# Performance work log

Hardware: AMD Instinct MI355X
Metric: run time of the kernel (lower is better)

Reference implementation:

```python
import jax, jax.numpy as jnp
import numpy as np

B, I, H = 512, 2048, 2048


def setup_inputs() -> dict:
    key = jax.random.key(0)
    ks = jax.random.split(key, 14)
    s = 0.02  # weight init scale
    inp = {
        "inputs": jax.random.normal(ks[0], (B, I), jnp.float32),
        "states": jax.random.normal(ks[1], (2, B, H), jnp.float32),
        "Wi": jax.random.normal(ks[2], (I, H), jnp.float32) * s,
        "Ui": jax.random.normal(ks[3], (H, H), jnp.float32) * s,
        "bi": jnp.zeros((H,), jnp.float32),
        "Wf": jax.random.normal(ks[4], (I, H), jnp.float32) * s,
        "Uf": jax.random.normal(ks[5], (H, H), jnp.float32) * s,
        "bf": jnp.zeros((H,), jnp.float32),
        "Wg": jax.random.normal(ks[6], (I, H), jnp.float32) * s,
        "Ug": jax.random.normal(ks[7], (H, H), jnp.float32) * s,
        "bg": jnp.zeros((H,), jnp.float32),
        "Wc": jax.random.normal(ks[8], (I, H), jnp.float32) * s,
        "Uc": jax.random.normal(ks[9], (H, H), jnp.float32) * s,
        "bc": jnp.zeros((H,), jnp.float32),
    }
    return inp


def reference(inputs, states, Wi, Ui, bi, Wf, Uf, bf, Wg, Ug, bg, Wc, Uc, bc):
    # Faithful to the original cell, including its quirks:
    # recurrent matmuls use states[0] (prevstate); c mixes states[1] (prevoutput).
    prevstate, prevoutput = states[0], states[1]  # [B,H] each
    i = jax.nn.sigmoid(inputs @ Wi + prevstate @ Ui + bi)
    f = jax.nn.sigmoid(inputs @ Wf + prevstate @ Uf + bf)
    g = jax.nn.sigmoid(inputs @ Wg + prevstate @ Ug + bg)
    c_ = jnp.tanh(inputs @ Wc + prevstate @ Uc + bc)
    c = f * prevoutput + i * c_
    state = g * jnp.tanh(c)
    return c, jnp.stack([state, c])
```

## Files before the change

### kernel.cpp

```cpp
#include <hip/hip_runtime.h>

#define BH (512*2048)
#define BHA 1048576ull
#define PPLANE (512ull*8192ull)
#define PLANE_BYTES (PPLANE*2ull)
#define AB_ELEMS (2ull*512*2048)

typedef __attribute__((ext_vector_type(8))) short short8;
typedef __attribute__((ext_vector_type(4))) float floatx4;
typedef __attribute__((ext_vector_type(4))) unsigned int uint4v;
typedef __attribute__((ext_vector_type(8))) unsigned short ushort8v;

__device__ inline unsigned pk2(float a, float b){
    unsigned ua = __builtin_bit_cast(unsigned, a) + 0x8000u;
    unsigned ub = __builtin_bit_cast(unsigned, b) + 0x8000u;
    return __builtin_amdgcn_perm(ub, ua, 0x07060302u);
}
__device__ inline unsigned short f2bf1(float x){
    return (unsigned short)((__builtin_bit_cast(unsigned, x) + 0x8000u) >> 16);
}
__device__ inline float bf2f(unsigned short s){
    return __builtin_bit_cast(float, ((unsigned)s) << 16);
}
__device__ inline int swz(int r, int g){ return r*4 + (g ^ ((r>>1)&3)); }
__device__ inline float fsig(float x){ return __builtin_amdgcn_rcpf(1.f + __expf(-x)); }
__device__ inline float ftanh(float x){ return 2.f*fsig(2.f*x) - 1.f; }

__global__ __launch_bounds__(256) void prep_act(
    const float* __restrict__ inputs, const float* __restrict__ states,
    unsigned short* __restrict__ Ab)
{
    const size_t off = ((size_t)blockIdx.x * 256 + threadIdx.x) * 8;
    const float* src = (off < BHA) ? (inputs + off) : (states + (off - BHA));
    floatx4 v0 = *(const floatx4*)src;
    floatx4 v1 = *(const floatx4*)(src + 4);
    uint4v w;
    w.x = pk2(v0[0],v0[1]); w.y = pk2(v0[2],v0[3]);
    w.z = pk2(v1[0],v1[1]); w.w = pk2(v1[2],v1[3]);
    *(uint4v*)(Ab + off) = w;
}

__global__ __launch_bounds__(256, 3) void gemm_fused(
    const float* __restrict__ Wi, const float* __restrict__ Ui,
    const float* __restrict__ Wf, const float* __restrict__ Uf,
    const float* __restrict__ Wg, const float* __restrict__ Ug,
    const float* __restrict__ Wc, const float* __restrict__ Uc,
    const unsigned short* __restrict__ Ab, unsigned short* __restrict__ P)
{
    __shared__ unsigned short As[2][4096];
    __shared__ unsigned short Bs[2][4096];

    const int t = threadIdx.x, lane = t & 63, wave = t >> 6;
    const int nblk = blockIdx.x, gate = nblk >> 4, nb = nblk & 15;
    const int m0 = blockIdx.y * 128, z = blockIdx.z;

    const float* Bsel;
    if (z < 2) { switch (gate){ case 0: Bsel=Wi; break; case 1: Bsel=Wf; break;
                                case 2: Bsel=Wg; break; default: Bsel=Wc; } }
    else       { switch (gate){ case 0: Bsel=Ui; break; case 1: Bsel=Uf; break;
                                case 2: Bsel=Ug; break; default: Bsel=Uc; } }
    const int n   = t & 127;
    const int o0  = t >> 7;
    const int swkB = (n >> 1) & 3;
    const float* Bp0 = Bsel + ((size_t)((z & 1) * 1024 + o0 * 8)) * 2048
                            + nb * 128 + n;
    const float* Bp1 = Bp0 + (size_t)16 * 2048;
    const int wb0 = n * 32 + (((o0    ) ^ swkB) << 3);
    const int wb1 = n * 32 + (((o0 + 2) ^ swkB) << 3);

    const int ar = t >> 1, ah = t & 1;
    const int swkA = (ar >> 1) & 3;
    const unsigned short* Aptr = Ab + (size_t)(z >> 1) * BHA
                               + (size_t)(m0 + ar) * 2048 + (z & 1) * 1024
                               + ah * 16;
    const int wa0 = ar * 32 + (((2*ah    ) ^ swkA) << 3);
    const int wa1 = ar * 32 + (((2*ah + 1) ^ swkA) << 3);

    floatx4 acc[4][4];
    #pragma unroll
    for (int i = 0; i < 4; i++)
        #pragma unroll
        for (int j = 0; j < 4; j++)
            acc[i][j] = (floatx4){0.f,0.f,0.f,0.f};

    const int wm = (wave & 1) * 64, wn = (wave >> 1) * 64;
    const int row16 = lane & 15, g4 = lane >> 4;
    const int fgx = ((g4 ^ ((row16 >> 1) & 3)) << 3);

    float uB0a[8], uB0b[8], uB1a[8], uB1b[8];
    uint4v uA0a, uA0b, uA1a, uA1b;

#define B_LOAD(d0, d1, tile) do { \
    const float* q0_ = Bp0 + (size_t)(tile) * 65536; \
    const float* q1_ = Bp1 + (size_t)(tile) * 65536; \
    _Pragma("unroll") for (int j = 0; j < 8; j++) d0[j] = q0_[(size_t)j * 2048]; \
    _Pragma("unroll") for (int j = 0; j < 8; j++) d1[j] = q1_[(size_t)j * 2048]; \
} while(0)

#define B_WRITE(buf, s0, s1) do { \
    *(uint4v*)&Bs[buf][wb0] = (uint4v){pk2(s0[0],s0[1]), pk2(s0[2],s0[3]), \
                                       pk2(s0[4],s0[5]), pk2(s0[6],s0[7])}; \
    *(uint4v*)&Bs[buf][wb1] = (uint4v){pk2(s1[0],s1[1]), pk2(s1[2],s1[3]), \
                                       pk2(s1[4],s1[5]), pk2(s1[6],s1[7])}; \
} while(0)

#define A_LOAD(da, db, tile) do { \
    const unsigned short* ap_ = Aptr + (size_t)(tile) * 32; \
    da = *(const uint4v*)ap_; db = *(const uint4v*)(ap_ + 8); \
} while(0)

#define A_WRITE(buf, sa, sb) do { \
    *(uint4v*)&As[buf][wa0] = sa; *(uint4v*)&As[buf][wa1] = sb; \
} while(0)

#define FRAGS_MFMA(buf) do { \
    short8 afr[4], bfr[4]; \
    _Pragma("unroll") for (int mi = 0; mi < 4; mi++) \
        afr[mi] = *(const short8*)&As[buf][(wm + mi*16 + row16)*32 + fgx]; \
    _Pragma("unroll") for (int ni = 0; ni < 4; ni++) \
        bfr[ni] = *(const short8*)&Bs[buf][(wn + ni*16 + row16)*32 + fgx]; \
    _Pragma("unroll") for (int mi = 0; mi < 4; mi++) \
        _Pragma("unroll") for (int ni = 0; ni < 4; ni++) \
            acc[mi][ni] = __builtin_amdgcn_mfma_f32_16x16x32_bf16( \
                afr[mi], bfr[ni], acc[mi][ni], 0, 0, 0); \
} while(0)

#define PIPE_BARRIER() do { \
    asm volatile("s_waitcnt lgkmcnt(0)" ::: "memory"); \
    __builtin_amdgcn_s_barrier(); \
    __builtin_amdgcn_sched_barrier(0); \
} while(0)

    A_LOAD(uA0a, uA0b, 0); B_LOAD(uB0a, uB0b, 0);
    A_LOAD(uA1a, uA1b, 1); B_LOAD(uB1a, uB1b, 1);
    A_WRITE(0, uA0a, uA0b);
    B_WRITE(0, uB0a, uB0b);
    PIPE_BARRIER();

    for (int kk = 0; kk < 32; kk += 2) {
        if (kk < 30) { A_LOAD(uA0a, uA0b, kk + 2); B_LOAD(uB0a, uB0b, kk + 2); }
        FRAGS_MFMA(0);
        A_WRITE(1, uA1a, uA1b);
        B_WRITE(1, uB1a, uB1b);
        PIPE_BARRIER();
        if (kk < 30) { A_LOAD(uA1a, uA1b, kk + 3); B_LOAD(uB1a, uB1b, kk + 3); }
        FRAGS_MFMA(1);
        if (kk < 30) {
            A_WRITE(0, uA0a, uA0b);
            B_WRITE(0, uB0a, uB0b);
        }
        PIPE_BARRIER();
    }

#undef B_LOAD
#undef B_WRITE
#undef A_LOAD
#undef A_WRITE
#undef FRAGS_MFMA
#undef PIPE_BARRIER

    unsigned short* dst = P + (size_t)z * PPLANE;
    const int gbase = gate * 2048 + nb * 128;
    #pragma unroll
    for (int mi = 0; mi < 4; mi++)
        #pragma unroll
        for (int ni = 0; ni < 4; ni++)
            #pragma unroll
            for (int j = 0; j < 4; j++) {
                int row = m0 + wm + mi*16 + g4*4 + j;
                int col = gbase + wn + ni*16 + row16;
                dst[(size_t)row * 8192 + col] = f2bf1(acc[mi][ni][j]);
            }
}

__global__ __launch_bounds__(256, 2) void gemm_tile(
    const float* __restrict__ inputs, const float* __restrict__ states,
    const float* __restrict__ Wi, const float* __restrict__ Ui,
    const float* __restrict__ Wf, const float* __restrict__ Uf,
    const float* __restrict__ Wg, const float* __restrict__ Ug,
    const float* __restrict__ Wc, const float* __restrict__ Uc,
    unsigned short* __restrict__ P, int KB)
{
    __shared__ uint4v As[2][512];
    __shared__ uint4v Bs[2][512];

    const int t = threadIdx.x;
    const int m0 = blockIdx.y * 128;
    const int z = blockIdx.z;
    const int nblk = blockIdx.x;
    const int gate = nblk >> 4;
    const int c0 = (nblk & 15) * 128;
    const int gk = z * KB;

    const float* Abase; const float* Bsel; int ko;
    if (gk < 2048) {
        Abase = inputs; ko = gk;
        switch (gate){ case 0: Bsel=Wi; break; case 1: Bsel=Wf; break;
                       case 2: Bsel=Wg; break; default: Bsel=Wc; }
    } else {
        Abase = states; ko = gk - 2048;
        switch (gate){ case 0: Bsel=Ui; break; case 1: Bsel=Uf; break;
                       case 2: Bsel=Ug; break; default: Bsel=Uc; }
    }
    const int NIT = KB >> 5;

    const int lane = t & 63, wave = t >> 6;
    const int wm = (wave & 1) * 64, wn = (wave >> 1) * 64;
    const int row16 = lane & 15, g4 = lane >> 4;
    const int ar = t >> 2, ag = t & 3;
    const int bn = t & 127, bg2 = (t >> 7) * 2;

    const float* Ap = Abase + (size_t)(m0 + ar) * 2048 + ko + ag * 8;
    const float* Bp = Bsel + (size_t)ko * 2048 + c0 + bn;

    floatx4 acc[4][4];
    #pragma unroll
    for (int i = 0; i < 4; i++)
        #pragma unroll
        for (int j = 0; j < 4; j++)
            acc[i][j] = (floatx4){0.f,0.f,0.f,0.f};

    floatx4 a0,a1,a2,a3; float b0[8], b1[8];
    a0 = *(const floatx4*)Ap;             a1 = *(const floatx4*)(Ap + 4);
    a2 = *(const floatx4*)(Ap + 64*2048); a3 = *(const floatx4*)(Ap + 64*2048 + 4);
    #pragma unroll
    for (int j = 0; j < 8; j++) b0[j] = Bp[(size_t)(bg2*8 + j) * 2048];
    #pragma unroll
    for (int j = 0; j < 8; j++) b1[j] = Bp[(size_t)(bg2*8 + 8 + j) * 2048];
    {
        uint4v w;
        w.x=pk2(a0[0],a0[1]); w.y=pk2(a0[2],a0[3]); w.z=pk2(a1[0],a1[1]); w.w=pk2(a1[2],a1[3]);
        As[0][swz(ar, ag)] = w;
        w.x=pk2(a2[0],a2[1]); w.y=pk2(a2[2],a2[3]); w.z=pk2(a3[0],a3[1]); w.w=pk2(a3[2],a3[3]);
        As[0][swz(ar+64, ag)] = w;
        w.x=pk2(b0[0],b0[1]); w.y=pk2(b0[2],b0[3]); w.z=pk2(b0[4],b0[5]); w.w=pk2(b0[6],b0[7]);
        Bs[0][swz(bn, bg2)] = w;
        w.x=pk2(b1[0],b1[1]); w.y=pk2(b1[2],b1[3]); w.z=pk2(b1[4],b1[5]); w.w=pk2(b1[6],b1[7]);
        Bs[0][swz(bn, bg2+1)] = w;
    }

    for (int kk = 0; kk < NIT; kk++) {
        __syncthreads();
        const int cur = kk & 1;
        if (kk + 1 < NIT) {
            const float* ap = Ap + (kk+1) * 32;
            a0 = *(const floatx4*)ap;             a1 = *(const floatx4*)(ap + 4);
            a2 = *(const floatx4*)(ap + 64*2048); a3 = *(const floatx4*)(ap + 64*2048 + 4);
            const float* bp = Bp + (size_t)(kk+1) * 32 * 2048;
            #pragma unroll
            for (int j = 0; j < 8; j++) b0[j] = bp[(size_t)(bg2*8 + j) * 2048];
            #pragma unroll
            for (int j = 0; j < 8; j++) b1[j] = bp[(size_t)(bg2*8 + 8 + j) * 2048];
        }
        short8 afr[4], bfr[4];
        #pragma unroll
        for (int mi = 0; mi < 4; mi++)
            afr[mi] = *(const short8*)&As[cur][swz(wm + mi*16 + row16, g4)];
        #pragma unroll
        for (int ni = 0; ni < 4; ni++)
            bfr[ni] = *(const short8*)&Bs[cur][swz(wn + ni*16 + row16, g4)];
        #pragma unroll
        for (int mi = 0; mi < 4; mi++)
            #pragma unroll
            for (int ni = 0; ni < 4; ni++)
                acc[mi][ni] = __builtin_amdgcn_mfma_f32_16x16x32_bf16(
                    afr[mi], bfr[ni], acc[mi][ni], 0, 0, 0);
        if (kk + 1 < NIT) {
            const int nxt = cur ^ 1;
            uint4v w;
            w.x=pk2(a0[0],a0[1]); w.y=pk2(a0[2],a0[3]); w.z=pk2(a1[0],a1[1]); w.w=pk2(a1[2],a1[3]);
            As[nxt][swz(ar, ag)] = w;
            w.x=pk2(a2[0],a2[1]); w.y=pk2(a2[2],a2[3]); w.z=pk2(a3[0],a3[1]); w.w=pk2(a3[2],a3[3]);
            As[nxt][swz(ar+64, ag)] = w;
            w.x=pk2(b0[0],b0[1]); w.y=pk2(b0[2],b0[3]); w.z=pk2(b0[4],b0[5]); w.w=pk2(b0[6],b0[7]);
            Bs[nxt][swz(bn, bg2)] = w;
            w.x=pk2(b1[0],b1[1]); w.y=pk2(b1[2],b1[3]); w.z=pk2(b1[4],b1[5]); w.w=pk2(b1[6],b1[7]);
            Bs[nxt][swz(bn, bg2+1)] = w;
        }
    }

    unsigned short* dst = P + (size_t)z * PPLANE;
    const int gbase = gate * 2048 + c0;
    #pragma unroll
    for (int mi = 0; mi < 4; mi++)
        #pragma unroll
        for (int ni = 0; ni < 4; ni++)
            #pragma unroll
            for (int j = 0; j < 4; j++) {
                int row = m0 + wm + mi*16 + g4*4 + j;
                int col = gbase + wn + ni*16 + row16;
                dst[(size_t)row * 8192 + col] = f2bf1(acc[mi][ni][j]);
            }
}

__global__ __launch_bounds__(256) void combine_kernel(
    float* __restrict__ out, const unsigned short* __restrict__ P,
    const float* __restrict__ states,
    const float* __restrict__ bi, const float* __restrict__ bfv,
    const float* __restrict__ bg, const float* __restrict__ bc, int nz)
{
    const int idx = (blockIdx.x * 256 + threadIdx.x) * 8;
    const int row = idx >> 11;
    const int h = idx & 2047;
    const size_t base = (size_t)row * 8192 + h;

    float xi[8], xf[8], xg[8], xc[8];
    #pragma unroll
    for (int e = 0; e < 8; e++) {
        xi[e] = bi[h+e]; xf[e] = bfv[h+e]; xg[e] = bg[h+e]; xc[e] = bc[h+e];
    }
    for (int z = 0; z < nz; z++) {
        const unsigned short* Pz = P + (size_t)z * PPLANE;
        ushort8v vi = *(const ushort8v*)&Pz[base];
        ushort8v vf = *(const ushort8v*)&Pz[base + 2048];
        ushort8v vg = *(const ushort8v*)&Pz[base + 4096];
        ushort8v vc = *(const ushort8v*)&Pz[base + 6144];
        #pragma unroll
        for (int e = 0; e < 8; e++) {
            xi[e] += bf2f(vi[e]); xf[e] += bf2f(vf[e]);
            xg[e] += bf2f(vg[e]); xc[e] += bf2f(vc[e]);
        }
    }

    const float* po = states + BH;
    floatx4 pov[2];
    pov[0] = *(const floatx4*)&po[idx];
    pov[1] = *(const floatx4*)&po[idx + 4];

    floatx4 vcv[2], vsv[2];
    #pragma unroll
    for (int q = 0; q < 2; q++)
        #pragma unroll
        for (int j = 0; j < 4; j++) {
            int e = q*4 + j;
            float c = fsig(xf[e]) * pov[q][j] + fsig(xi[e]) * ftanh(xc[e]);
            vcv[q][j] = c;
            vsv[q][j] = fsig(xg[e]) * ftanh(c);
        }
    #pragma unroll
    for (int q = 0; q < 2; q++) {
        *(floatx4*)&out[idx + q*4]        = vcv[q];
        *(floatx4*)&out[BH + idx + q*4]   = vsv[q];
        *(floatx4*)&out[2*BH + idx + q*4] = vcv[q];
    }
}

extern "C" void kernel_launch(void* const* d_in, const int* in_sizes, int n_in,
                              void* d_out, int out_size, void* d_ws, size_t ws_size,
                              hipStream_t stream) {
    const float* inputs = (const float*)d_in[0];
    const float* states = (const float*)d_in[1];
    const float* Wi = (const float*)d_in[2];
    const float* Ui = (const float*)d_in[3];
    const float* bi = (const float*)d_in[4];
    const float* Wf = (const float*)d_in[5];
    const float* Uf = (const float*)d_in[6];
    const float* bf = (const float*)d_in[7];
    const float* Wg = (const float*)d_in[8];
    const float* Ug = (const float*)d_in[9];
    const float* bg = (const float*)d_in[10];
    const float* Wc = (const float*)d_in[11];
    const float* Uc = (const float*)d_in[12];
    const float* bc = (const float*)d_in[13];
    float* out = (float*)d_out;

    const size_t need = (AB_ELEMS + 4 * PPLANE) * 2;
    if (ws_size >= need) {
        unsigned short* Ab = (unsigned short*)d_ws;
        unsigned short* P  = Ab + AB_ELEMS;
        prep_act<<<1024, 256, 0, stream>>>(inputs, states, Ab);
        gemm_fused<<<dim3(64, 4, 4), 256, 0, stream>>>(Wi, Ui, Wf, Uf,
                                                       Wg, Ug, Wc, Uc, Ab, P);
        combine_kernel<<<BH / (8 * 256), 256, 0, stream>>>(out, P, states,
                                                           bi, bf, bg, bc, 4);
    } else {
        unsigned short* P = (unsigned short*)d_ws;
        const int nz = (ws_size >= 4 * PLANE_BYTES) ? 4 : 2;
        const int KB = 4096 / nz;
        dim3 grid(64, 4, nz);
        gemm_tile<<<grid, 256, 0, stream>>>(inputs, states, Wi, Ui, Wf, Uf,
                                            Wg, Ug, Wc, Uc, P, KB);
        combine_kernel<<<BH / (8 * 256), 256, 0, stream>>>(out, P, states,
                                                           bi, bf, bg, bc, nz);
    }
}
```

Before: 238.2 us.

## Load A fragments directly from global and widen B loads to float2

Removes the shared-memory staging of the A (activation) tile: each wave now reads its MFMA A-fragments directly from global memory into registers, double-buffered across k-steps. B loads become float2 vectors covering two columns per thread, with a new swizzled LDS write layout. Launch bounds drop from 3 to 2 blocks per CU to make room for the extra registers. The aim is to cut LDS traffic and halve B load instructions. The cost is that A rows are now fetched redundantly by the two waves sharing the same wm, and occupancy is lower.

```diff
diff --git a/kernel.cpp b/kernel.cpp
--- a/kernel.cpp
+++ b/kernel.cpp
@@ -8,6 +8,7 @@
 
 typedef __attribute__((ext_vector_type(8))) short short8;
 typedef __attribute__((ext_vector_type(4))) float floatx4;
+typedef __attribute__((ext_vector_type(2))) float floatx2;
 typedef __attribute__((ext_vector_type(4))) unsigned int uint4v;
 typedef __attribute__((ext_vector_type(8))) unsigned short ushort8v;
 
@@ -40,41 +41,40 @@
     *(uint4v*)(Ab + off) = w;
 }
 
-__global__ __launch_bounds__(256, 3) void gemm_fused(
+__global__ __launch_bounds__(256, 2) void gemm_fused(
     const float* __restrict__ Wi, const float* __restrict__ Ui,
     const float* __restrict__ Wf, const float* __restrict__ Uf,
     const float* __restrict__ Wg, const float* __restrict__ Ug,
     const float* __restrict__ Wc, const float* __restrict__ Uc,
     const unsigned short* __restrict__ Ab, unsigned short* __restrict__ P)
 {
-    __shared__ unsigned short As[2][4096];
     __shared__ unsigned short Bs[2][4096];
 
     const int t = threadIdx.x, lane = t & 63, wave = t >> 6;
-    const int nblk = blockIdx.x, gate = nblk >> 4, nb = nblk & 15;
+    const int nblk = blockIdx.x, gate = nblk >> 4, nbx = nblk & 15;
     const int m0 = blockIdx.y * 128, z = blockIdx.z;
+    const int ko = (z & 1) * 1024;
 
     const float* Bsel;
     if (z < 2) { switch (gate){ case 0: Bsel=Wi; break; case 1: Bsel=Wf; break;
                                 case 2: Bsel=Wg; break; default: Bsel=Wc; } }
     else       { switch (gate){ case 0: Bsel=Ui; break; case 1: Bsel=Uf; break;
                                 case 2: Bsel=Ug; break; default: Bsel=Uc; } }
-    const int n   = t & 127;
-    const int o0  = t >> 7;
-    const int swkB = (n >> 1) & 3;
-    const float* Bp0 = Bsel + ((size_t)((z & 1) * 1024 + o0 * 8)) * 2048
-                            + nb * 128 + n;
-    const float* Bp1 = Bp0 + (size_t)16 * 2048;
-    const int wb0 = n * 32 + (((o0    ) ^ swkB) << 3);
-    const int wb1 = n * 32 + (((o0 + 2) ^ swkB) << 3);
-
-    const int ar = t >> 1, ah = t & 1;
-    const int swkA = (ar >> 1) & 3;
-    const unsigned short* Aptr = Ab + (size_t)(z >> 1) * BHA
-                               + (size_t)(m0 + ar) * 2048 + (z & 1) * 1024
-                               + ah * 16;
-    const int wa0 = ar * 32 + (((2*ah    ) ^ swkA) << 3);
-    const int wa1 = ar * 32 + (((2*ah + 1) ^ swkA) << 3);
+
+    const int n0  = lane * 2;
+    const int oct = wave;
+    const float* Bp = Bsel + (size_t)(ko + oct * 8) * 2048 + nbx * 128 + n0;
+    const int keyB = lane & 3;
+    const int wb0 = n0 * 32 + ((oct ^ keyB) << 3);
+    const int wb1 = wb0 + 32;
+
+    const int wm = (wave & 1) * 64, wn = (wave >> 1) * 64;
+    const int row16 = lane & 15, g4 = lane >> 4;
+    const int fgx = (g4 ^ ((row16 >> 1) & 3)) << 3;
+
+    const unsigned short* Ap = Ab + (size_t)(z >> 1) * BHA
+                             + (size_t)(m0 + wm + row16) * 2048
+                             + (z & 1) * 1024 + g4 * 8;
 
     floatx4 acc[4][4];
     #pragma unroll
@@ -83,84 +83,73 @@
         for (int j = 0; j < 4; j++)
             acc[i][j] = (floatx4){0.f,0.f,0.f,0.f};
 
-    const int wm = (wave & 1) * 64, wn = (wave >> 1) * 64;
-    const int row16 = lane & 15, g4 = lane >> 4;
-    const int fgx = ((g4 ^ ((row16 >> 1) & 3)) << 3);
-
-    float uB0a[8], uB0b[8], uB1a[8], uB1b[8];
-    uint4v uA0a, uA0b, uA1a, uA1b;
-
-#define B_LOAD(d0, d1, tile) do { \
-    const float* q0_ = Bp0 + (size_t)(tile) * 65536; \
-    const float* q1_ = Bp1 + (size_t)(tile) * 65536; \
-    _Pragma("unroll") for (int j = 0; j < 8; j++) d0[j] = q0_[(size_t)j * 2048]; \
-    _Pragma("unroll") for (int j = 0; j < 8; j++) d1[j] = q1_[(size_t)j * 2048]; \
-} while(0)
-
-#define B_WRITE(buf, s0, s1) do { \
-    *(uint4v*)&Bs[buf][wb0] = (uint4v){pk2(s0[0],s0[1]), pk2(s0[2],s0[3]), \
-                                       pk2(s0[4],s0[5]), pk2(s0[6],s0[7])}; \
-    *(uint4v*)&Bs[buf][wb1] = (uint4v){pk2(s1[0],s1[1]), pk2(s1[2],s1[3]), \
-                                       pk2(s1[4],s1[5]), pk2(s1[6],s1[7])}; \
-} while(0)
-
-#define A_LOAD(da, db, tile) do { \
-    const unsigned short* ap_ = Aptr + (size_t)(tile) * 32; \
-    da = *(const uint4v*)ap_; db = *(const uint4v*)(ap_ + 8); \
-} while(0)
-
-#define A_WRITE(buf, sa, sb) do { \
-    *(uint4v*)&As[buf][wa0] = sa; *(uint4v*)&As[buf][wa1] = sb; \
-} while(0)
-
-#define FRAGS_MFMA(buf) do { \
-    short8 afr[4], bfr[4]; \
+    floatx2 q0[8], q1[8];
+    short8 fA[4], fB[4];
+
+#define B_LOAD(d, tile) do { \
+    const float* bp_ = Bp + (size_t)(tile) * 65536; \
+    _Pragma("unroll") for (int j = 0; j < 8; j++) \
+        d[j] = *(const floatx2*)(bp_ + (size_t)j * 2048); \
+} while(0)
+
+#define B_WRITE(buf, s) do { \
+    *(uint4v*)&Bs[buf][wb0] = (uint4v){pk2(s[0].x,s[1].x), pk2(s[2].x,s[3].x), \
+                                       pk2(s[4].x,s[5].x), pk2(s[6].x,s[7].x)}; \
+    *(uint4v*)&Bs[buf][wb1] = (uint4v){pk2(s[0].y,s[1].y), pk2(s[2].y,s[3].y), \
+                                       pk2(s[4].y,s[5].y), pk2(s[6].y,s[7].y)}; \
+} while(0)
+
+#define A_LOADF(f, tile) do { \
     _Pragma("unroll") for (int mi = 0; mi < 4; mi++) \
-        afr[mi] = *(const short8*)&As[buf][(wm + mi*16 + row16)*32 + fgx]; \
+        f[mi] = *(const short8*)(Ap + (size_t)mi * 32768 + (size_t)(tile) * 32); \
+} while(0)
+
+#define MFMA_STEP(buf, f) do { \
+    short8 bfr[4]; \
     _Pragma("unroll") for (int ni = 0; ni < 4; ni++) \
         bfr[ni] = *(const short8*)&Bs[buf][(wn + ni*16 + row16)*32 + fgx]; \
     _Pragma("unroll") for (int mi = 0; mi < 4; mi++) \
         _Pragma("unroll") for (int ni = 0; ni < 4; ni++) \
             acc[mi][ni] = __builtin_amdgcn_mfma_f32_16x16x32_bf16( \
-                afr[mi], bfr[ni], acc[mi][ni], 0, 0, 0); \
-} while(0)
-
-#define PIPE_BARRIER() do { \
+                f[mi], bfr[ni], acc[mi][ni], 0, 0, 0); \
+} while(0)
+
+#define PIPEBAR() do { \
     asm volatile("s_waitcnt lgkmcnt(0)" ::: "memory"); \
     __builtin_amdgcn_s_barrier(); \
     __builtin_amdgcn_sched_barrier(0); \
 } while(0)
 
-    A_LOAD(uA0a, uA0b, 0); B_LOAD(uB0a, uB0b, 0);
-    A_LOAD(uA1a, uA1b, 1); B_LOAD(uB1a, uB1b, 1);
-    A_WRITE(0, uA0a, uA0b);
-    B_WRITE(0, uB0a, uB0b);
-    PIPE_BARRIER();
+    B_LOAD(q0, 0);
+    B_LOAD(q1, 1);
+    A_LOADF(fA, 0);
+    A_LOADF(fB, 1);
+    B_WRITE(0, q0);
+    PIPEBAR();
 
     for (int kk = 0; kk < 32; kk += 2) {
-        if (kk < 30) { A_LOAD(uA0a, uA0b, kk + 2); B_LOAD(uB0a, uB0b, kk + 2); }
-        FRAGS_MFMA(0);
-        A_WRITE(1, uA1a, uA1b);
-        B_WRITE(1, uB1a, uB1b);
-        PIPE_BARRIER();
-        if (kk < 30) { A_LOAD(uA1a, uA1b, kk + 3); B_LOAD(uB1a, uB1b, kk + 3); }
-        FRAGS_MFMA(1);
+        if (kk < 30) B_LOAD(q0, kk + 2);
+        MFMA_STEP(0, fA);
+        B_WRITE(1, q1);
+        if (kk < 30) A_LOADF(fA, kk + 2);
+        PIPEBAR();
+        if (kk < 30) B_LOAD(q1, kk + 3);
+        MFMA_STEP(1, fB);
         if (kk < 30) {
-            A_WRITE(0, uA0a, uA0b);
-            B_WRITE(0, uB0a, uB0b);
-        }
-        PIPE_BARRIER();
+            B_WRITE(0, q0);
+            A_LOADF(fB, kk + 3);
+        }
+        PIPEBAR();
     }
 
 #undef B_LOAD
 #undef B_WRITE
-#undef A_LOAD
-#undef A_WRITE
-#undef FRAGS_MFMA
-#undef PIPE_BARRIER
+#undef A_LOADF
+#undef MFMA_STEP
+#undef PIPEBAR
 
     unsigned short* dst = P + (size_t)z * PPLANE;
-    const int gbase = gate * 2048 + nb * 128;
+    const int gbase = gate * 2048 + nbx * 128;
     #pragma unroll
     for (int mi = 0; mi < 4; mi++)
         #pragma unroll
```

Result: slower. 267.1 us (+12.1%).
